# Performance work log

Hardware: AMD Instinct MI355X
Metric: run time of the kernel (lower is better)

The kernel has to match this reference:

```python
import jax, jax.numpy as jnp
import numpy as np

N = 262144          # total sentence instances
H = 256             # encoder hidden_dim
C = 128             # class_count
NUM_BAGS = 8192     # number of bags (segments)


def setup_inputs() -> dict:
    key = jax.random.key(0)
    k1, k2, k3, k4 = jax.random.split(key, 4)
    hidden = jax.random.normal(k1, (N, H), dtype=jnp.float32)
    W = jax.random.normal(k2, (C, H), dtype=jnp.float32) * 0.02
    b = jax.random.normal(k3, (C,), dtype=jnp.float32) * 0.02
    bag_id = jnp.sort(jax.random.randint(k4, (N,), 0, NUM_BAGS, dtype=jnp.int64))
    return {"hidden": hidden, "W": W, "b": b, "bag_id": bag_id}


def reference(hidden, W, b, bag_id):
    # Segment mean over bags (replaces the Python loop: hidden[bag_id == id].mean(0))
    sums = jax.ops.segment_sum(hidden, bag_id, num_segments=NUM_BAGS)          # [NUM_BAGS, H]
    counts = jax.ops.segment_sum(jnp.ones((hidden.shape[0],), hidden.dtype),
                                 bag_id, num_segments=NUM_BAGS)                # [NUM_BAGS]
    mean_hidden = sums / jnp.maximum(counts, 1.0)[:, None]                     # [NUM_BAGS, H]
    # classifier: nn.Linear(hidden_dim, class_count)
    select_logits = jnp.einsum('gh,ch->gc', mean_hidden, W) + b               # [NUM_BAGS, C]
    return select_logits
```

## Files before the change

### kernel.cpp

```cpp
#include <hip/hip_runtime.h>


#define NBAGS 8192
#define HDIM 256
#define CDIM 128
#define BPB 8

__global__ __launch_bounds__(256) void bagre_kernel(
    const float* __restrict__ hidden,
    const float* __restrict__ W,
    const float* __restrict__ b,
    const int* __restrict__ bag_id,
    float* __restrict__ out,
    int N)
{
    __shared__ __align__(16) float s_mean[BPB][HDIM];
    __shared__ float s_part[2][BPB][CDIM];
    __shared__ int s_bound[BPB + 1];

    const int t  = threadIdx.x;
    const int g0 = blockIdx.x * BPB;

    if (t <= BPB) {
        const int target = g0 + t;
        int lo = 0, hi = N;
        while (lo < hi) {
            const int mid = (lo + hi) >> 1;
            if (bag_id[mid] < target) lo = mid + 1; else hi = mid;
        }
        s_bound[t] = lo;
    }
    __syncthreads();

    const int q    = t >> 6;
    const int lane = t & 63;
    const int col4 = lane << 2;

#pragma unroll
    for (int jj = 0; jj < 2; ++jj) {
        const int j = q * 2 + jj;
        const int s = s_bound[j];
        const int e = s_bound[j + 1];

        float4 a0 = make_float4(0.f, 0.f, 0.f, 0.f);
        float4 a1 = a0, a2 = a0, a3 = a0;

        const float* __restrict__ p = hidden + (size_t)s * HDIM + col4;
        int r = s;
        for (; r + 4 <= e; r += 4, p += 4 * HDIM) {
            const float4 v0 = *(const float4*)(p + 0 * HDIM);
            const float4 v1 = *(const float4*)(p + 1 * HDIM);
            const float4 v2 = *(const float4*)(p + 2 * HDIM);
            const float4 v3 = *(const float4*)(p + 3 * HDIM);
            a0.x += v0.x; a0.y += v0.y; a0.z += v0.z; a0.w += v0.w;
            a1.x += v1.x; a1.y += v1.y; a1.z += v1.z; a1.w += v1.w;
            a2.x += v2.x; a2.y += v2.y; a2.z += v2.z; a2.w += v2.w;
            a3.x += v3.x; a3.y += v3.y; a3.z += v3.z; a3.w += v3.w;
        }
        for (; r < e; ++r, p += HDIM) {
            const float4 v0 = *(const float4*)p;
            a0.x += v0.x; a0.y += v0.y; a0.z += v0.z; a0.w += v0.w;
        }

        const int cnt = e - s;
        const float inv = 1.0f / (float)(cnt > 1 ? cnt : 1);
        float4 m;
        m.x = (a0.x + a1.x + a2.x + a3.x) * inv;
        m.y = (a0.y + a1.y + a2.y + a3.y) * inv;
        m.z = (a0.z + a1.z + a2.z + a3.z) * inv;
        m.w = (a0.w + a1.w + a2.w + a3.w) * inv;
        *(float4*)(&s_mean[j][col4]) = m;
    }
    __syncthreads();

    const int c    = t & (CDIM - 1);
    const int half = t >> 7;
    const float* __restrict__ wrow = W + (size_t)c * HDIM + half * (HDIM / 2);

    float acc[BPB];
#pragma unroll
    for (int j = 0; j < BPB; ++j) acc[j] = 0.f;

    for (int hh = 0; hh < HDIM / 2; hh += 4) {
        const float4 wv = *(const float4*)(wrow + hh);
        const int hbase = half * (HDIM / 2) + hh;
#pragma unroll
        for (int j = 0; j < BPB; ++j) {
            acc[j] += s_mean[j][hbase + 0] * wv.x
                    + s_mean[j][hbase + 1] * wv.y
                    + s_mean[j][hbase + 2] * wv.z
                    + s_mean[j][hbase + 3] * wv.w;
        }
    }

#pragma unroll
    for (int j = 0; j < BPB; ++j) s_part[half][j][c] = acc[j];
    __syncthreads();

    for (int idx = t; idx < BPB * CDIM; idx += 256) {
        const int j  = idx >> 7;
        const int cc = idx & (CDIM - 1);
        out[(size_t)(g0 + j) * CDIM + cc] =
            s_part[0][j][cc] + s_part[1][j][cc] + b[cc];
    }
}

extern "C" void kernel_launch(void* const* d_in, const int* in_sizes, int n_in,
                              void* d_out, int out_size, void* d_ws, size_t ws_size,
                              hipStream_t stream) {
    const float* hidden = (const float*)d_in[0];
    const float* W      = (const float*)d_in[1];
    const float* b      = (const float*)d_in[2];
    const int*   bag_id = (const int*)d_in[3];
    float* out = (float*)d_out;
    const int N = in_sizes[3];

    bagre_kernel<<<NBAGS / BPB, 256, 0, stream>>>(hidden, W, b, bag_id, out, N);
}
```

Before: 387.5 us.

## Split fused bag-mean and classifier into two kernels via workspace

Splits the single fused kernel into a segment-mean kernel and a separate GEMV-style logits kernel, with the means passed through a workspace buffer in global memory. The mean kernel now gives each wavefront one bag, finds its bounds with per-lane binary search and wave shuffles, and needs no shared memory or block barriers. It launches more, smaller blocks with a higher occupancy hint. The aim is to raise occupancy and overlap on the memory-bound reduction. In exchange it adds a second launch and a write and reread of the 8 MB means array.

```diff
diff --git a/kernel.cpp b/kernel.cpp
--- a/kernel.cpp
+++ b/kernel.cpp
@@ -4,105 +4,98 @@
 #define NBAGS 8192
 #define HDIM 256
 #define CDIM 128
-#define BPB 8
 
-__global__ __launch_bounds__(256) void bagre_kernel(
+__global__ __launch_bounds__(256, 8) void bag_mean_kernel(
     const float* __restrict__ hidden,
-    const float* __restrict__ W,
-    const float* __restrict__ b,
     const int* __restrict__ bag_id,
-    float* __restrict__ out,
+    float* __restrict__ means,
     int N)
 {
-    __shared__ __align__(16) float s_mean[BPB][HDIM];
-    __shared__ float s_part[2][BPB][CDIM];
-    __shared__ int s_bound[BPB + 1];
+    const int q    = threadIdx.x >> 6;
+    const int lane = threadIdx.x & 63;
+    const int bag  = blockIdx.x * 4 + q;
 
-    const int t  = threadIdx.x;
-    const int g0 = blockIdx.x * BPB;
-
-    if (t <= BPB) {
-        const int target = g0 + t;
+    int bound = 0;
+    if (lane < 2) {
+        const int target = bag + lane;
         int lo = 0, hi = N;
         while (lo < hi) {
             const int mid = (lo + hi) >> 1;
             if (bag_id[mid] < target) lo = mid + 1; else hi = mid;
         }
-        s_bound[t] = lo;
+        bound = lo;
     }
-    __syncthreads();
+    const int s = __shfl(bound, 0);
+    const int e = __shfl(bound, 1);
 
-    const int q    = t >> 6;
-    const int lane = t & 63;
     const int col4 = lane << 2;
+    float4 a0 = make_float4(0.f, 0.f, 0.f, 0.f);
+    float4 a1 = a0, a2 = a0, a3 = a0;
 
-#pragma unroll
-    for (int jj = 0; jj < 2; ++jj) {
-        const int j = q * 2 + jj;
-        const int s = s_bound[j];
-        const int e = s_bound[j + 1];
-
-        float4 a0 = make_float4(0.f, 0.f, 0.f, 0.f);
-        float4 a1 = a0, a2 = a0, a3 = a0;
-
-        const float* __restrict__ p = hidden + (size_t)s * HDIM + col4;
-        int r = s;
-        for (; r + 4 <= e; r += 4, p += 4 * HDIM) {
-            const float4 v0 = *(const float4*)(p + 0 * HDIM);
-            const float4 v1 = *(const float4*)(p + 1 * HDIM);
-            const float4 v2 = *(const float4*)(p + 2 * HDIM);
-            const float4 v3 = *(const float4*)(p + 3 * HDIM);
-            a0.x += v0.x; a0.y += v0.y; a0.z += v0.z; a0.w += v0.w;
-            a1.x += v1.x; a1.y += v1.y; a1.z += v1.z; a1.w += v1.w;
-            a2.x += v2.x; a2.y += v2.y; a2.z += v2.z; a2.w += v2.w;
-            a3.x += v3.x; a3.y += v3.y; a3.z += v3.z; a3.w += v3.w;
-        }
-        for (; r < e; ++r, p += HDIM) {
-            const float4 v0 = *(const float4*)p;
-            a0.x += v0.x; a0.y += v0.y; a0.z += v0.z; a0.w += v0.w;
-        }
-
-        const int cnt = e - s;
-        const float inv = 1.0f / (float)(cnt > 1 ? cnt : 1);
-        float4 m;
-        m.x = (a0.x + a1.x + a2.x + a3.x) * inv;
-        m.y = (a0.y + a1.y + a2.y + a3.y) * inv;
-        m.z = (a0.z + a1.z + a2.z + a3.z) * inv;
-        m.w = (a0.w + a1.w + a2.w + a3.w) * inv;
-        *(float4*)(&s_mean[j][col4]) = m;
+    const float* __restrict__ p = hidden + (size_t)s * HDIM + col4;
+    int r = s;
+    for (; r + 4 <= e; r += 4, p += 4 * HDIM) {
+        const float4 v0 = *(const float4*)(p + 0 * HDIM);
+        const float4 v1 = *(const float4*)(p + 1 * HDIM);
+        const float4 v2 = *(const float4*)(p + 2 * HDIM);
+        const float4 v3 = *(const float4*)(p + 3 * HDIM);
+        a0.x += v0.x; a0.y += v0.y; a0.z += v0.z; a0.w += v0.w;
+        a1.x += v1.x; a1.y += v1.y; a1.z += v1.z; a1.w += v1.w;
+        a2.x += v2.x; a2.y += v2.y; a2.z += v2.z; a2.w += v2.w;
+        a3.x += v3.x; a3.y += v3.y; a3.z += v3.z; a3.w += v3.w;
     }
-    __syncthreads();
-
-    const int c    = t & (CDIM - 1);
-    const int half = t >> 7;
-    const float* __restrict__ wrow = W + (size_t)c * HDIM + half * (HDIM / 2);
-
-    float acc[BPB];
-#pragma unroll
-    for (int j = 0; j < BPB; ++j) acc[j] = 0.f;
-
-    for (int hh = 0; hh < HDIM / 2; hh += 4) {
-        const float4 wv = *(const float4*)(wrow + hh);
-        const int hbase = half * (HDIM / 2) + hh;
-#pragma unroll
-        for (int j = 0; j < BPB; ++j) {
-            acc[j] += s_mean[j][hbase + 0] * wv.x
-                    + s_mean[j][hbase + 1] * wv.y
-                    + s_mean[j][hbase + 2] * wv.z
-                    + s_mean[j][hbase + 3] * wv.w;
-        }
+    for (; r < e; ++r, p += HDIM) {
+        const float4 v0 = *(const float4*)p;
+        a0.x += v0.x; a0.y += v0.y; a0.z += v0.z; a0.w += v0.w;
     }
 
-#pragma unroll
-    for (int j = 0; j < BPB; ++j) s_part[half][j][c] = acc[j];
-    __syncthreads();
+    const int cnt = e - s;
+    const float inv = 1.0f / (float)(cnt > 1 ? cnt : 1);
+    float4 m;
+    m.x = (a0.x + a1.x + a2.x + a3.x) * inv;
+    m.y = (a0.y + a1.y + a2.y + a3.y) * inv;
+    m.z = (a0.z + a1.z + a2.z + a3.z) * inv;
+    m.w = (a0.w + a1.w + a2.w + a3.w) * inv;
+    *(float4*)(means + (size_t)bag * HDIM + col4) = m;
+}
 
-    for (int idx = t; idx < BPB * CDIM; idx += 256) {
-        const int j  = idx >> 7;
-        const int cc = idx & (CDIM - 1);
-        out[(size_t)(g0 + j) * CDIM + cc] =
-            s_part[0][j][cc] + s_part[1][j][cc] + b[cc];
+__global__ __launch_bounds__(256) void bag_logits_kernel(
+    const float* __restrict__ means,
+    const float* __restrict__ W,
+    const float* __restrict__ b,
+    float* __restrict__ out)
+{
+    const int t  = threadIdx.x;
+    const int g0 = blockIdx.x * 8;
+    const int c  = t & (CDIM - 1);
+    const int jg = t >> 7;
+    const int j0 = jg * 4;
+
+    const float* __restrict__ wrow = W + (size_t)c * HDIM;
+    const float* __restrict__ m0 = means + (size_t)(g0 + j0 + 0) * HDIM;
+    const float* __restrict__ m1 = means + (size_t)(g0 + j0 + 1) * HDIM;
+    const float* __restrict__ m2 = means + (size_t)(g0 + j0 + 2) * HDIM;
+    const float* __restrict__ m3 = means + (size_t)(g0 + j0 + 3) * HDIM;
+
+    float acc0 = 0.f, acc1 = 0.f, acc2 = 0.f, acc3 = 0.f;
+#pragma unroll 4
+    for (int k = 0; k < HDIM; k += 4) {
+        const float4 wv = *(const float4*)(wrow + k);
+        const float4 u0 = *(const float4*)(m0 + k);
+        const float4 u1 = *(const float4*)(m1 + k);
+        const float4 u2 = *(const float4*)(m2 + k);
+        const float4 u3 = *(const float4*)(m3 + k);
+        acc0 += u0.x * wv.x + u0.y * wv.y + u0.z * wv.z + u0.w * wv.w;
+        acc1 += u1.x * wv.x + u1.y * wv.y + u1.z * wv.z + u1.w * wv.w;
+        acc2 += u2.x * wv.x + u2.y * wv.y + u2.z * wv.z + u2.w * wv.w;
+        acc3 += u3.x * wv.x + u3.y * wv.y + u3.z * wv.z + u3.w * wv.w;
     }
+
+    const float bias = b[c];
+    out[(size_t)(g0 + j0 + 0) * CDIM + c] = acc0 + bias;
+    out[(size_t)(g0 + j0 + 1) * CDIM + c] = acc1 + bias;
+    out[(size_t)(g0 + j0 + 2) * CDIM + c] = acc2 + bias;
+    out[(size_t)(g0 + j0 + 3) * CDIM + c] = acc3 + bias;
 }
 
 extern "C" void kernel_launch(void* const* d_in, const int* in_sizes, int n_in,
@@ -112,8 +105,10 @@
     const float* W      = (const float*)d_in[1];
     const float* b      = (const float*)d_in[2];
     const int*   bag_id = (const int*)d_in[3];
-    float* out = (float*)d_out;
+    float* out   = (float*)d_out;
+    float* means = (float*)d_ws;
     const int N = in_sizes[3];
 
-    bagre_kernel<<<NBAGS / BPB, 256, 0, stream>>>(hidden, W, b, bag_id, out, N);
+    bag_mean_kernel<<<NBAGS / 4, 256, 0, stream>>>(hidden, bag_id, means, N);
+    bag_logits_kernel<<<NBAGS / 8, 256, 0, stream>>>(means, W, b, out);
 }
```

After: 433.1 us. +11.8%, slower.

## Split fused bag-mean and classifier into two kernels with LDS-staged W

Applied to the files above, without the earlier changes.

Splits the fused kernel into a segment-mean kernel that writes bag means to workspace and a separate logits kernel. The logits kernel stages half of W (64 rows) in swizzled LDS per block and has each wave compute two bags, reading means straight from global memory. The aim is to stop the per-block GEMV from reading W out of global memory and sitting serialized behind the memory-bound reduction. In exchange it adds a second launch, an 8 MB round trip of means through global memory, and a W reload into 64 KB of LDS for every block, which limits occupancy.

```diff
diff --git a/kernel.cpp b/kernel.cpp
--- a/kernel.cpp
+++ b/kernel.cpp
@@ -4,24 +4,18 @@
 #define NBAGS 8192
 #define HDIM 256
 #define CDIM 128
-#define BPB 8
 
-__global__ __launch_bounds__(256) void bagre_kernel(
+__global__ __launch_bounds__(256) void bag_mean_kernel(
     const float* __restrict__ hidden,
-    const float* __restrict__ W,
-    const float* __restrict__ b,
     const int* __restrict__ bag_id,
-    float* __restrict__ out,
+    float* __restrict__ means,
     int N)
 {
-    __shared__ __align__(16) float s_mean[BPB][HDIM];
-    __shared__ float s_part[2][BPB][CDIM];
-    __shared__ int s_bound[BPB + 1];
+    __shared__ int s_bound[9];
+    const int t  = threadIdx.x;
+    const int g0 = blockIdx.x * 8;
 
-    const int t  = threadIdx.x;
-    const int g0 = blockIdx.x * BPB;
-
-    if (t <= BPB) {
+    if (t <= 8) {
         const int target = g0 + t;
         int lo = 0, hi = N;
         while (lo < hi) {
@@ -69,40 +63,58 @@
         m.y = (a0.y + a1.y + a2.y + a3.y) * inv;
         m.z = (a0.z + a1.z + a2.z + a3.z) * inv;
         m.w = (a0.w + a1.w + a2.w + a3.w) * inv;
-        *(float4*)(&s_mean[j][col4]) = m;
+        *(float4*)(means + (size_t)(g0 + j) * HDIM + col4) = m;
+    }
+}
+
+__global__ __launch_bounds__(256) void bag_logits_kernel(
+    const float* __restrict__ means,
+    const float* __restrict__ W,
+    const float* __restrict__ b,
+    float* __restrict__ out)
+{
+    __shared__ float wlds[64 * HDIM];
+
+    const int t     = threadIdx.x;
+    const int chalf = blockIdx.x & 1;
+    const int g0    = (blockIdx.x >> 1) * 8;
+
+    {
+        const float* __restrict__ src = W + (size_t)chalf * 64 * HDIM;
+#pragma unroll
+        for (int i = 0; i < 16; ++i) {
+            const int fi = i * 256 + t;
+            const int f  = fi << 2;
+            const int cl = f >> 8;
+            const int k  = f & 255;
+            const float4 v = *(const float4*)(src + f);
+            *(float4*)(&wlds[cl * HDIM + (k ^ ((cl & 7) << 2))]) = v;
+        }
     }
     __syncthreads();
 
-    const int c    = t & (CDIM - 1);
-    const int half = t >> 7;
-    const float* __restrict__ wrow = W + (size_t)c * HDIM + half * (HDIM / 2);
+    const int wv   = t >> 6;
+    const int lane = t & 63;
+    const int cg   = chalf * 64 + lane;
 
-    float acc[BPB];
-#pragma unroll
-    for (int j = 0; j < BPB; ++j) acc[j] = 0.f;
+    const float* __restrict__ m0 = means + (size_t)(g0 + 2 * wv) * HDIM;
+    const float* __restrict__ m1 = m0 + HDIM;
+    const float* __restrict__ wrow = wlds + lane * HDIM;
+    const int sw = (lane & 7) << 2;
 
-    for (int hh = 0; hh < HDIM / 2; hh += 4) {
-        const float4 wv = *(const float4*)(wrow + hh);
-        const int hbase = half * (HDIM / 2) + hh;
-#pragma unroll
-        for (int j = 0; j < BPB; ++j) {
-            acc[j] += s_mean[j][hbase + 0] * wv.x
-                    + s_mean[j][hbase + 1] * wv.y
-                    + s_mean[j][hbase + 2] * wv.z
-                    + s_mean[j][hbase + 3] * wv.w;
-        }
+    float acc0 = 0.f, acc1 = 0.f;
+#pragma unroll 4
+    for (int k = 0; k < HDIM; k += 4) {
+        const float4 wv4 = *(const float4*)(wrow + (k ^ sw));
+        const float4 u0  = *(const float4*)(m0 + k);
+        const float4 u1  = *(const float4*)(m1 + k);
+        acc0 += u0.x * wv4.x + u0.y * wv4.y + u0.z * wv4.z + u0.w * wv4.w;
+        acc1 += u1.x * wv4.x + u1.y * wv4.y + u1.z * wv4.z + u1.w * wv4.w;
     }
 
-#pragma unroll
-    for (int j = 0; j < BPB; ++j) s_part[half][j][c] = acc[j];
-    __syncthreads();
-
-    for (int idx = t; idx < BPB * CDIM; idx += 256) {
-        const int j  = idx >> 7;
-        const int cc = idx & (CDIM - 1);
-        out[(size_t)(g0 + j) * CDIM + cc] =
-            s_part[0][j][cc] + s_part[1][j][cc] + b[cc];
-    }
+    const float bias = b[cg];
+    out[(size_t)(g0 + 2 * wv)     * CDIM + cg] = acc0 + bias;
+    out[(size_t)(g0 + 2 * wv + 1) * CDIM + cg] = acc1 + bias;
 }
 
 extern "C" void kernel_launch(void* const* d_in, const int* in_sizes, int n_in,
@@ -112,8 +124,10 @@
     const float* W      = (const float*)d_in[1];
     const float* b      = (const float*)d_in[2];
     const int*   bag_id = (const int*)d_in[3];
-    float* out = (float*)d_out;
+    float* out   = (float*)d_out;
+    float* means = (float*)d_ws;
     const int N = in_sizes[3];
 
-    bagre_kernel<<<NBAGS / BPB, 256, 0, stream>>>(hidden, W, b, bag_id, out, N);
+    bag_mean_kernel<<<NBAGS / 8, 256, 0, stream>>>(hidden, bag_id, means, N);
+    bag_logits_kernel<<<(NBAGS / 8) * 2, 256, 0, stream>>>(means, W, b, out);
 }
```

New measurement: 409.9 us. 5.8% more time.
